# Kernel tuning notes

Hardware: AMD Instinct MI355X
Metric: run time of the kernel (lower is better)

## Reference

```python
import jax, jax.numpy as jnp
import numpy as np

HIDDEN = 2048
HEADS = 16
HEAD_DIM = HIDDEN // HEADS
NEG = -10000000000.0

def setup_inputs() -> dict:
    key = jax.random.key(0)
    k1, k2, k3 = jax.random.split(key, 3)
    x = jax.random.normal(k1, (2, 2048, HIDDEN), dtype=jnp.float32)
    # Dense kernels (flax convention: y = x @ W), lecun_normal-ish scaling
    w_qkv = jax.random.normal(k2, (HIDDEN, 3 * HIDDEN), dtype=jnp.float32) / np.sqrt(HIDDEN)
    w_out = jax.random.normal(k3, (HIDDEN, HIDDEN), dtype=jnp.float32) / np.sqrt(HIDDEN)
    return {"x": x, "w_qkv": w_qkv, "w_out": w_out}

def reference(x, w_qkv, w_out):
    b, s, _ = x.shape
    qkv = x @ w_qkv  # [b, s, 3*hidden]
    qkv = qkv.reshape(b, s, 3, HEADS, HEAD_DIM)
    q, k, v = qkv[:, :, 0], qkv[:, :, 1], qkv[:, :, 2]
    scale = jnp.sqrt(jnp.float32(HEAD_DIM)).astype(x.dtype)
    q = q / scale
    scores = jnp.einsum('bqhd,bkhd->bhqk', q, k)  # [b, h, s, s]
    causal_mask = jnp.arange(s)[:, None] >= jnp.arange(s)[None, :]
    scores = jnp.where(causal_mask[None, None], scores, NEG)
    attn = jax.nn.softmax(scores, axis=-1)
    out = jnp.einsum('bhqk,bkhd->bqhd', attn, v).reshape(b, s, HIDDEN)
    return out @ w_out
```

## Files before the change

### kernel.cpp

```cpp
#include <hip/hip_runtime.h>
#include <hip/hip_bf16.h>

typedef __attribute__((ext_vector_type(8))) short bf16x8;
typedef __attribute__((ext_vector_type(4))) float f32x4;
typedef unsigned short ushort_t;

#define HID 2048
#define QKVN 6144
#define SEQ 2048
#define NH 16
#define HD 128
#define QB 128
#define KVB 64

#define GLOBAL_AS __attribute__((address_space(1)))
#define LDS_AS __attribute__((address_space(3)))
typedef LDS_AS const char lds_char;

__device__ __forceinline__ void gload_lds16(const ushort_t* g, ushort_t* l) {
    __builtin_amdgcn_global_load_lds((const GLOBAL_AS unsigned int*)g,
                                     (LDS_AS unsigned int*)l, 16, 0, 0);
}

__device__ __forceinline__ bf16x8 dsr128(lds_char* p) {
    bf16x8 r;
    asm volatile("ds_read_b128 %0, %1" : "=v"(r) : "v"(p));
    return r;
}

__device__ __forceinline__ ushort_t f2b(float f) {
    union { float f; unsigned int u; } x; x.f = f;
    unsigned int r = x.u + 0x7fffu + ((x.u >> 16) & 1u);
    return (ushort_t)(r >> 16);
}

#define BARX() asm volatile("s_barrier" ::: "memory")
#define LGKM0() asm volatile("s_waitcnt lgkmcnt(0)" ::: "memory")
#define VMC6() asm volatile("s_waitcnt vmcnt(6)" ::: "memory")
#define VMC0() asm volatile("s_waitcnt vmcnt(0)" ::: "memory")

__global__ __launch_bounds__(256) void castbf(const float* __restrict__ in,
                                              ushort_t* __restrict__ out, int n) {
    int i = (blockIdx.x * 256 + threadIdx.x) * 8;
    if (i >= n) return;
    float4 a = *(const float4*)(in + i);
    float4 b = *(const float4*)(in + i + 4);
    union { ushort_t u[8]; uint4 v; } r;
    r.u[0] = f2b(a.x); r.u[1] = f2b(a.y); r.u[2] = f2b(a.z); r.u[3] = f2b(a.w);
    r.u[4] = f2b(b.x); r.u[5] = f2b(b.y); r.u[6] = f2b(b.z); r.u[7] = f2b(b.w);
    *(uint4*)(out + i) = r.v;
}

__global__ __launch_bounds__(256) void transcast(const float* __restrict__ in,
                                                 ushort_t* __restrict__ out,
                                                 int Kd, int Nd) {
    __shared__ float tile[32][33];
    int tx = threadIdx.x & 31, ty = threadIdx.x >> 5;
    int n0 = blockIdx.x * 32, k0 = blockIdx.y * 32;
    for (int j = 0; j < 4; j++)
        tile[ty + 8 * j][tx] = in[(size_t)(k0 + ty + 8 * j) * Nd + n0 + tx];
    __syncthreads();
    for (int j = 0; j < 4; j++)
        out[(size_t)(n0 + ty + 8 * j) * Kd + k0 + tx] = f2b(tile[tx][ty + 8 * j]);
}

__global__ __launch_bounds__(256) void transV(const ushort_t* __restrict__ qkvb,
                                              ushort_t* __restrict__ vT) {
    __shared__ ushort_t tile[32][33];
    int tx = threadIdx.x & 31, ty = threadIdx.x >> 5;
    int s0 = blockIdx.x * 32, d0 = blockIdx.y * 32;
    int bh = blockIdx.z; int b = bh >> 4, h = bh & 15;
    for (int j = 0; j < 4; j++)
        tile[ty + 8 * j][tx] =
            qkvb[(size_t)(b * SEQ + s0 + ty + 8 * j) * QKVN + 2 * HID + h * HD + d0 + tx];
    __syncthreads();
    for (int j = 0; j < 4; j++)
        vT[((size_t)bh * HD + d0 + ty + 8 * j) * SEQ + s0 + tx] = tile[tx][ty + 8 * j];
}

template <bool OUT_BF16>
__global__ __launch_bounds__(512, 1) void gemm4p(const ushort_t* __restrict__ A,
                                                 const ushort_t* __restrict__ BT,
                                                 void* __restrict__ C,
                                                 int M, int N, int K,
                                                 int scale_cols, float scale) {
    __shared__ __align__(16) ushort_t As[2][2][128 * 32];
    __shared__ __align__(16) ushort_t Bs[2][2][256 * 32];

    const int t = threadIdx.x;
    const int l = t & 63, w = t >> 6;
    const int wm = w >> 2, wn = w & 3;
    const int lr = l & 15, lg = l >> 4;

    const int nwg = gridDim.x;
    const int cpx = nwg >> 3;
    const int swb = (blockIdx.x & 7) * cpx + (blockIdx.x >> 3);
    const int NTN = N >> 8;
    const int m0 = (swb / NTN) << 7, n0 = (swb % NTN) << 8;

    const int NKT = K >> 6;
    const int NIT = NKT >> 1;

    f32x4 acc[4][4] = {};

#define STAGE_A(BUF, KK, KT)                                                    \
    do {                                                                        \
        const int r_ = t >> 2, g_ = t & 3;                                      \
        const int gc_ = ((KT) << 6) + ((KK) << 5) + ((g_ ^ (r_ & 3)) << 3);     \
        gload_lds16(A + (size_t)(m0 + r_) * K + gc_, &As[BUF][KK][t * 8]);      \
    } while (0)
#define STAGE_B(BUF, KK, KT)                                                        \
    do {                                                                            \
        _Pragma("unroll") for (int sx = 0; sx < 2; sx++) {                          \
            const int i_ = sx * 512 + t;                                            \
            const int r_ = i_ >> 2, g_ = i_ & 3;                                    \
            const int gc_ = ((KT) << 6) + ((KK) << 5) + ((g_ ^ (r_ & 3)) << 3);     \
            gload_lds16(BT + (size_t)(n0 + r_) * K + gc_, &Bs[BUF][KK][i_ * 8]);    \
        }                                                                           \
    } while (0)

#define PHASE(BUF, KK, STAGES)                                                  \
    {                                                                           \
        bf16x8 af[4], bfr[4];                                                   \
        lds_char* aB_ = (lds_char*)&As[BUF][KK][0];                             \
        lds_char* bB_ = (lds_char*)&Bs[BUF][KK][0];                             \
        const int co_ = (lg ^ (lr & 3)) << 4;                                   \
        _Pragma("unroll") for (int mi = 0; mi < 4; mi++)                        \
            af[mi] = dsr128(aB_ + (wm * 64 + mi * 16 + lr) * 64 + co_);         \
        _Pragma("unroll") for (int nn = 0; nn < 4; nn++)                        \
            bfr[nn] = dsr128(bB_ + (wn * 64 + nn * 16 + lr) * 64 + co_);        \
        STAGES;                                                                 \
        VMC6();                                                                 \
        BARX();                                                                 \
        LGKM0();                                                                \
        __builtin_amdgcn_sched_barrier(0);                                      \
        __builtin_amdgcn_s_setprio(1);                                          \
        _Pragma("unroll") for (int mi = 0; mi < 4; mi++)                        \
            _Pragma("unroll") for (int nn = 0; nn < 4; nn++)                    \
                acc[mi][nn] = __builtin_amdgcn_mfma_f32_16x16x32_bf16(          \
                    af[mi], bfr[nn], acc[mi][nn], 0, 0, 0);                     \
        __builtin_amdgcn_s_setprio(0);                                          \
        BARX();                                                                 \
    }

    STAGE_A(0, 0, 0); STAGE_B(0, 0, 0);
    STAGE_A(0, 1, 0); STAGE_B(0, 1, 0);
    STAGE_A(1, 0, 1); STAGE_B(1, 0, 1);
    VMC6();
    BARX();

    for (int it = 0; it < NIT; it++) {
        const int kt1 = 2 * it + 1;
        const int kt2 = min(2 * it + 2, NKT - 1);
        const int kt3 = min(2 * it + 3, NKT - 1);
        PHASE(0, 0, { STAGE_A(1, 1, kt1); STAGE_B(1, 1, kt1); });
        PHASE(0, 1, { STAGE_A(0, 0, kt2); STAGE_B(0, 0, kt2); });
        PHASE(1, 0, { STAGE_A(0, 1, kt2); STAGE_B(0, 1, kt2); });
        PHASE(1, 1, { STAGE_A(1, 0, kt3); STAGE_B(1, 0, kt3); });
    }
    VMC0();

#undef PHASE
#undef STAGE_A
#undef STAGE_B

#pragma unroll
    for (int mi = 0; mi < 4; mi++)
#pragma unroll
        for (int nn = 0; nn < 4; nn++) {
            const int row = m0 + wm * 64 + mi * 16 + lg * 4;
            const int col = n0 + wn * 64 + nn * 16 + lr;
            const float sc = (col < scale_cols) ? scale : 1.0f;
            const f32x4 v = acc[mi][nn];
#pragma unroll
            for (int j = 0; j < 4; j++) {
                if (OUT_BF16)
                    ((ushort_t*)C)[(size_t)(row + j) * N + col] = f2b(v[j] * sc);
                else
                    ((float*)C)[(size_t)(row + j) * N + col] = v[j] * sc;
            }
        }
}

__global__ __launch_bounds__(512, 1) void attn_fwd3(const ushort_t* __restrict__ qkvb,
                                                    const ushort_t* __restrict__ vT,
                                                    ushort_t* __restrict__ attnb) {
    __shared__ __align__(16) ushort_t Ks[2][64 * 128];
    __shared__ __align__(16) ushort_t Vs[2][128 * 64];
    __shared__ __align__(16) ushort_t Ps[8][16 * 64];

    const int t = threadIdx.x;
    const int l = t & 63, w = t >> 6;
    const int lr = l & 15, lg = l >> 4;
    const int pr = blockIdx.x, h = blockIdx.y, b = blockIdx.z;

    const ushort_t* kg = qkvb + (size_t)(b * SEQ) * QKVN + HID + h * HD;
    const ushort_t* vg = vT + (size_t)(b * NH + h) * HD * SEQ;

    char* PsB = (char*)Ps[w];
    const int pssz = ((lr & 7) ^ ((lr >> 3) << 1)) << 4;

    const int kcA = 2 * w, kcB = 2 * w + 1;
    const int krA = 8 * w + (l >> 4), krB = krA + 4;
    const int kcolA = ((l & 15) ^ (l >> 4)) << 3;
    const int kcolB = ((l & 15) ^ (4 + (l >> 4))) << 3;
    const int vrA = 16 * w + (l >> 3), vrB = vrA + 8;
    const int vcol = ((l & 7) ^ (l >> 3)) << 3;

    for (int seg = 0; seg < 2; seg++) {
        const int qt = (seg == 0) ? pr : 15 - pr;
        const int q0 = qt * QB;
        const int q0w = q0 + w * 16;
        const int NT = (q0 + QB) / KVB;

        bf16x8 qf[4];
        {
            const ushort_t* qb = qkvb + (size_t)(b * SEQ + q0w + lr) * QKVN + h * HD + lg * 8;
#pragma unroll
            for (int kc = 0; kc < 4; kc++) qf[kc] = *(const bf16x8*)(qb + kc * 32);
        }
        f32x4 o[8] = {};
        float m[4] = {-3e38f, -3e38f, -3e38f, -3e38f};
        float ls[4] = {0.f, 0.f, 0.f, 0.f};

        __syncthreads();
        gload_lds16(kg + (size_t)krA * QKVN + kcolA, &Ks[0][kcA * 512 + l * 8]);
        gload_lds16(kg + (size_t)krB * QKVN + kcolB, &Ks[0][kcB * 512 + l * 8]);
        gload_lds16(vg + (size_t)vrA * SEQ + vcol,   &Vs[0][kcA * 512 + l * 8]);
        gload_lds16(vg + (size_t)vrB * SEQ + vcol,   &Vs[0][kcB * 512 + l * 8]);

        for (int kt = 0; kt < NT; kt++) {
            const int kv0 = kt * KVB;
            __syncthreads();
            if (kt + 1 < NT) {
                const int nb = (kt + 1) & 1;
                const int nkv = kv0 + KVB;
                gload_lds16(kg + (size_t)(nkv + krA) * QKVN + kcolA, &Ks[nb][kcA * 512 + l * 8]);
                gload_lds16(kg + (size_t)(nkv + krB) * QKVN + kcolB, &Ks[nb][kcB * 512 + l * 8]);
                gload_lds16(vg + (size_t)vrA * SEQ + nkv + vcol,     &Vs[nb][kcA * 512 + l * 8]);
                gload_lds16(vg + (size_t)vrB * SEQ + nkv + vcol,     &Vs[nb][kcB * 512 + l * 8]);
            }
            if (kv0 > q0w + 15) continue;
            const char* KsB = (const char*)Ks[kt & 1];
            const char* VsB = (const char*)Vs[kt & 1];

            f32x4 s[4];
            const int rs = (lr & 7) << 4;
#pragma unroll
            for (int nf = 0; nf < 4; nf++) {
                const int r = nf * 16 + lr;
                s[nf] = (f32x4){0.f, 0.f, 0.f, 0.f};
#pragma unroll
                for (int kc = 0; kc < 4; kc++) {
                    bf16x8 kf = *(const bf16x8*)(KsB + r * 256 + ((kc * 64 + lg * 16) ^ rs));
                    s[nf] = __builtin_amdgcn_mfma_f32_16x16x32_bf16(qf[kc], kf, s[nf], 0, 0, 0);
                }
            }

            const bool diag = (kv0 + 63 > q0w);
            float tm[4];
#pragma unroll
            for (int j = 0; j < 4; j++) {
                if (diag) {
                    const int qpos = q0w + lg * 4 + j;
#pragma unroll
                    for (int nf = 0; nf < 4; nf++)
                        if (kv0 + nf * 16 + lr > qpos) s[nf][j] = -3e38f;
                }
                tm[j] = fmaxf(fmaxf(s[0][j], s[1][j]), fmaxf(s[2][j], s[3][j]));
#pragma unroll
                for (int mk = 1; mk < 16; mk <<= 1)
                    tm[j] = fmaxf(tm[j], __shfl_xor(tm[j], mk, 64));
            }

            float grow = fmaxf(fmaxf(tm[0] - m[0], tm[1] - m[1]),
                               fmaxf(tm[2] - m[2], tm[3] - m[3]));
            if (!__all(grow <= 8.0f)) {
#pragma unroll
                for (int j = 0; j < 4; j++) {
                    const float mn = fmaxf(m[j], tm[j]);
                    const float fac = exp2f((m[j] - mn) * 1.44269504f);
                    m[j] = mn; ls[j] *= fac;
#pragma unroll
                    for (int nf2 = 0; nf2 < 8; nf2++) o[nf2][j] *= fac;
                }
            }

#pragma unroll
            for (int j = 0; j < 4; j++) {
                const int row = lg * 4 + j;
                const int rsz = ((row & 7) ^ ((row >> 3) << 1)) << 4;
                float psum = 0.f;
#pragma unroll
                for (int nf = 0; nf < 4; nf++) {
                    float p = exp2f((s[nf][j] - m[j]) * 1.44269504f);
                    psum += p;
                    union { float f; unsigned u; } cv; cv.f = p;
                    *(ushort_t*)(PsB + row * 128 + ((nf * 32 + lr * 2) ^ rsz)) = (ushort_t)(cv.u >> 16);
                }
                ls[j] += psum;
            }

            bf16x8 pa0 = *(const bf16x8*)(PsB + lr * 128 + ((lg * 16) ^ pssz));
            bf16x8 pa1 = *(const bf16x8*)(PsB + lr * 128 + ((64 + lg * 16) ^ pssz));
#pragma unroll
            for (int nf2 = 0; nf2 < 8; nf2++) {
                const int vr2 = nf2 * 16 + lr;
                bf16x8 vb0 = *(const bf16x8*)(VsB + vr2 * 128 + ((lg * 16) ^ rs));
                bf16x8 vb1 = *(const bf16x8*)(VsB + vr2 * 128 + ((64 + lg * 16) ^ rs));
                o[nf2] = __builtin_amdgcn_mfma_f32_16x16x32_bf16(pa0, vb0, o[nf2], 0, 0, 0);
                o[nf2] = __builtin_amdgcn_mfma_f32_16x16x32_bf16(pa1, vb1, o[nf2], 0, 0, 0);
            }
        }

        float inv[4];
#pragma unroll
        for (int j = 0; j < 4; j++) {
            float sum = ls[j];
#pragma unroll
            for (int mk = 1; mk < 16; mk <<= 1) sum += __shfl_xor(sum, mk, 64);
            inv[j] = 1.0f / sum;
        }
        ushort_t* ob = attnb + (size_t)(b * SEQ + q0w) * HID + h * HD;
#pragma unroll
        for (int nf2 = 0; nf2 < 8; nf2++)
#pragma unroll
            for (int j = 0; j < 4; j++)
                ob[(size_t)(lg * 4 + j) * HID + nf2 * 16 + lr] = f2b(o[nf2][j] * inv[j]);
    }
}

extern "C" void kernel_launch(void* const* d_in, const int* in_sizes, int n_in,
                              void* d_out, int out_size, void* d_ws, size_t ws_size,
                              hipStream_t stream) {
    const float* x     = (const float*)d_in[0];
    const float* w_qkv = (const float*)d_in[1];
    const float* w_out = (const float*)d_in[2];
    float* out = (float*)d_out;

    char* ws = (char*)d_ws;
    ushort_t* xb    = (ushort_t*)(ws);
    ushort_t* wqkvT = (ushort_t*)(ws + 16777216);
    ushort_t* woutT = (ushort_t*)(ws + 41943040);
    ushort_t* qkvb  = (ushort_t*)(ws + 50331648);
    ushort_t* vT    = (ushort_t*)(ws + 100663296);
    ushort_t* attnb = (ushort_t*)(ws + 117440512);

    const int M = 2 * SEQ;

    castbf<<<(M * HID) / (256 * 8), 256, 0, stream>>>(x, xb, M * HID);
    transcast<<<dim3(QKVN / 32, HID / 32), 256, 0, stream>>>(w_qkv, wqkvT, HID, QKVN);
    transcast<<<dim3(HID / 32, HID / 32), 256, 0, stream>>>(w_out, woutT, HID, HID);

    gemm4p<true><<<(M / 128) * (QKVN / 256), 512, 0, stream>>>(
        xb, wqkvT, qkvb, M, QKVN, HID, HID, 0.08838834764831845f);

    transV<<<dim3(SEQ / 32, HD / 32, 2 * NH), 256, 0, stream>>>(qkvb, vT);

    attn_fwd3<<<dim3(8, NH, 2), 512, 0, stream>>>(qkvb, vT, attnb);

    gemm4p<false><<<(M / 128) * (HID / 256), 512, 0, stream>>>(
        attnb, woutT, out, M, HID, HID, 0, 1.0f);
}
```

Baseline: 282.9 us.

## Rewrite GEMM as triple-buffered register-prefetch pipeline with wider QKV tile

Replaces the two-stage, double-k-half GEMM with a three-slot LDS ring over 32-wide K steps. LDS fragment reads for the next step go into alternate register sets while the current step's MFMAs run, and each step issues only one barrier. The swizzle pattern is changed, and the QKV projection uses 384-wide N tiles (6 fragments per wave) to cut the tile count and raise reuse of A. This adds register pressure and LDS use, and the grid count for QKV (32*16=512 tiles) changes how evenly work spreads across CUs.

Measured after the change: 269.1 us. 1.05x faster.

```diff
diff --git a/kernel.cpp b/kernel.cpp
--- a/kernel.cpp
+++ b/kernel.cpp
@@ -36,7 +36,6 @@
 
 #define BARX() asm volatile("s_barrier" ::: "memory")
 #define LGKM0() asm volatile("s_waitcnt lgkmcnt(0)" ::: "memory")
-#define VMC6() asm volatile("s_waitcnt vmcnt(6)" ::: "memory")
 #define VMC0() asm volatile("s_waitcnt vmcnt(0)" ::: "memory")
 
 __global__ __launch_bounds__(256) void castbf(const float* __restrict__ in,
@@ -78,14 +77,14 @@
         vT[((size_t)bh * HD + d0 + ty + 8 * j) * SEQ + s0 + tx] = tile[tx][ty + 8 * j];
 }
 
-template <bool OUT_BF16>
-__global__ __launch_bounds__(512, 1) void gemm4p(const ushort_t* __restrict__ A,
+template <int NFRAG, bool OUT_BF16>
+__global__ __launch_bounds__(512, 1) void gemmpl(const ushort_t* __restrict__ A,
                                                  const ushort_t* __restrict__ BT,
                                                  void* __restrict__ C,
                                                  int M, int N, int K,
                                                  int scale_cols, float scale) {
-    __shared__ __align__(16) ushort_t As[2][2][128 * 32];
-    __shared__ __align__(16) ushort_t Bs[2][2][256 * 32];
+    __shared__ __align__(16) ushort_t As[3][128 * 32];
+    __shared__ __align__(16) ushort_t Bs[3][NFRAG * 64 * 32];
 
     const int t = threadIdx.x;
     const int l = t & 63, w = t >> 6;
@@ -95,83 +94,107 @@
     const int nwg = gridDim.x;
     const int cpx = nwg >> 3;
     const int swb = (blockIdx.x & 7) * cpx + (blockIdx.x >> 3);
-    const int NTN = N >> 8;
-    const int m0 = (swb / NTN) << 7, n0 = (swb % NTN) << 8;
-
-    const int NKT = K >> 6;
-    const int NIT = NKT >> 1;
-
-    f32x4 acc[4][4] = {};
-
-#define STAGE_A(BUF, KK, KT)                                                    \
+    const int BN = NFRAG * 64;
+    const int NTN = N / BN;
+    const int m0 = (swb / NTN) << 7, n0 = (swb % NTN) * BN;
+
+    const int NKT = K >> 5;
+
+    f32x4 acc[4][NFRAG] = {};
+    bf16x8 afA[4], bfA[NFRAG], afB[4], bfB[NFRAG];
+
+#define VMCL()                                                                      \
+    do { if constexpr (NFRAG == 6) asm volatile("s_waitcnt vmcnt(4)" ::: "memory"); \
+         else                      asm volatile("s_waitcnt vmcnt(3)" ::: "memory"); } while (0)
+#define VMC2L()                                                                     \
+    do { if constexpr (NFRAG == 6) asm volatile("s_waitcnt vmcnt(8)" ::: "memory"); \
+         else                      asm volatile("s_waitcnt vmcnt(6)" ::: "memory"); } while (0)
+
+#define STAGE_A(BUF, KT)                                                        \
     do {                                                                        \
         const int r_ = t >> 2, g_ = t & 3;                                      \
-        const int gc_ = ((KT) << 6) + ((KK) << 5) + ((g_ ^ (r_ & 3)) << 3);     \
-        gload_lds16(A + (size_t)(m0 + r_) * K + gc_, &As[BUF][KK][t * 8]);      \
+        const int gc_ = ((KT) << 5) + ((g_ ^ ((r_ >> 1) & 3)) << 3);            \
+        gload_lds16(A + (size_t)(m0 + r_) * K + gc_, &As[BUF][t * 8]);          \
     } while (0)
-#define STAGE_B(BUF, KK, KT)                                                        \
+#define STAGE_B(BUF, KT)                                                        \
+    do {                                                                        \
+        _Pragma("unroll") for (int sx = 0; sx < NFRAG / 2; sx++) {              \
+            const int i_ = sx * 512 + t;                                        \
+            const int r_ = i_ >> 2, g_ = i_ & 3;                                \
+            const int gc_ = ((KT) << 5) + ((g_ ^ ((r_ >> 1) & 3)) << 3);        \
+            gload_lds16(BT + (size_t)(n0 + r_) * K + gc_, &Bs[BUF][i_ * 8]);    \
+        }                                                                       \
+    } while (0)
+
+#define READS(AF, BF, BI)                                                           \
     do {                                                                            \
-        _Pragma("unroll") for (int sx = 0; sx < 2; sx++) {                          \
-            const int i_ = sx * 512 + t;                                            \
-            const int r_ = i_ >> 2, g_ = i_ & 3;                                    \
-            const int gc_ = ((KT) << 6) + ((KK) << 5) + ((g_ ^ (r_ & 3)) << 3);     \
-            gload_lds16(BT + (size_t)(n0 + r_) * K + gc_, &Bs[BUF][KK][i_ * 8]);    \
-        }                                                                           \
+        lds_char* aB_ = (lds_char*)&As[BI][0];                                      \
+        lds_char* bB_ = (lds_char*)&Bs[BI][0];                                      \
+        const int co_ = (lg ^ ((lr >> 1) & 3)) << 4;                                \
+        _Pragma("unroll") for (int mi = 0; mi < 4; mi++)                            \
+            AF[mi] = dsr128(aB_ + (wm * 64 + mi * 16 + lr) * 64 + co_);             \
+        _Pragma("unroll") for (int nj = 0; nj < NFRAG; nj++)                        \
+            BF[nj] = dsr128(bB_ + (wn * (NFRAG * 16) + nj * 16 + lr) * 64 + co_);   \
     } while (0)
 
-#define PHASE(BUF, KK, STAGES)                                                  \
+#define MFMAS(AF, BF)                                                           \
+    do {                                                                        \
+        __builtin_amdgcn_s_setprio(1);                                          \
+        _Pragma("unroll") for (int mi = 0; mi < 4; mi++)                        \
+            _Pragma("unroll") for (int nj = 0; nj < NFRAG; nj++)                \
+                acc[mi][nj] = __builtin_amdgcn_mfma_f32_16x16x32_bf16(          \
+                    AF[mi], BF[nj], acc[mi][nj], 0, 0, 0);                      \
+        __builtin_amdgcn_s_setprio(0);                                          \
+    } while (0)
+
+#define STEPX(AFU, BFU, AFV, BFV, BI, KT)                                       \
     {                                                                           \
-        bf16x8 af[4], bfr[4];                                                   \
-        lds_char* aB_ = (lds_char*)&As[BUF][KK][0];                             \
-        lds_char* bB_ = (lds_char*)&Bs[BUF][KK][0];                             \
-        const int co_ = (lg ^ (lr & 3)) << 4;                                   \
-        _Pragma("unroll") for (int mi = 0; mi < 4; mi++)                        \
-            af[mi] = dsr128(aB_ + (wm * 64 + mi * 16 + lr) * 64 + co_);         \
-        _Pragma("unroll") for (int nn = 0; nn < 4; nn++)                        \
-            bfr[nn] = dsr128(bB_ + (wn * 64 + nn * 16 + lr) * 64 + co_);        \
-        STAGES;                                                                 \
-        VMC6();                                                                 \
-        BARX();                                                                 \
         LGKM0();                                                                \
         __builtin_amdgcn_sched_barrier(0);                                      \
-        __builtin_amdgcn_s_setprio(1);                                          \
-        _Pragma("unroll") for (int mi = 0; mi < 4; mi++)                        \
-            _Pragma("unroll") for (int nn = 0; nn < 4; nn++)                    \
-                acc[mi][nn] = __builtin_amdgcn_mfma_f32_16x16x32_bf16(          \
-                    af[mi], bfr[nn], acc[mi][nn], 0, 0, 0);                     \
-        __builtin_amdgcn_s_setprio(0);                                          \
         BARX();                                                                 \
+        int nb_ = (BI) + 1; if (nb_ == 3) nb_ = 0;                              \
+        READS(AFV, BFV, nb_);                                                   \
+        const int st_ = min((KT) + 3, NKT - 1);                                 \
+        STAGE_A(BI, st_);                                                       \
+        STAGE_B(BI, st_);                                                       \
+        VMCL();                                                                 \
+        __builtin_amdgcn_sched_barrier(0);                                      \
+        MFMAS(AFU, BFU);                                                        \
     }
 
-    STAGE_A(0, 0, 0); STAGE_B(0, 0, 0);
-    STAGE_A(0, 1, 0); STAGE_B(0, 1, 0);
-    STAGE_A(1, 0, 1); STAGE_B(1, 0, 1);
-    VMC6();
+    STAGE_A(0, 0); STAGE_B(0, 0);
+    STAGE_A(1, 1); STAGE_B(1, 1);
+    STAGE_A(2, 2); STAGE_B(2, 2);
+    VMC2L();
     BARX();
-
-    for (int it = 0; it < NIT; it++) {
-        const int kt1 = 2 * it + 1;
-        const int kt2 = min(2 * it + 2, NKT - 1);
-        const int kt3 = min(2 * it + 3, NKT - 1);
-        PHASE(0, 0, { STAGE_A(1, 1, kt1); STAGE_B(1, 1, kt1); });
-        PHASE(0, 1, { STAGE_A(0, 0, kt2); STAGE_B(0, 0, kt2); });
-        PHASE(1, 0, { STAGE_A(0, 1, kt2); STAGE_B(0, 1, kt2); });
-        PHASE(1, 1, { STAGE_A(1, 0, kt3); STAGE_B(1, 0, kt3); });
+    READS(afA, bfA, 0);
+    VMCL();
+
+    int bi = 0;
+    for (int kt = 0; kt < NKT; kt += 2) {
+        STEPX(afA, bfA, afB, bfB, bi, kt);
+        int bi1 = bi + 1; if (bi1 == 3) bi1 = 0;
+        STEPX(afB, bfB, afA, bfA, bi1, kt + 1);
+        bi += 2; if (bi >= 3) bi -= 3;
     }
     VMC0();
 
-#undef PHASE
+#undef STEPX
+#undef MFMAS
+#undef READS
 #undef STAGE_A
 #undef STAGE_B
+#undef VMCL
+#undef VMC2L
 
 #pragma unroll
     for (int mi = 0; mi < 4; mi++)
 #pragma unroll
-        for (int nn = 0; nn < 4; nn++) {
+        for (int nj = 0; nj < NFRAG; nj++) {
             const int row = m0 + wm * 64 + mi * 16 + lg * 4;
-            const int col = n0 + wn * 64 + nn * 16 + lr;
+            const int col = n0 + wn * (NFRAG * 16) + nj * 16 + lr;
             const float sc = (col < scale_cols) ? scale : 1.0f;
-            const f32x4 v = acc[mi][nn];
+            const f32x4 v = acc[mi][nj];
 #pragma unroll
             for (int j = 0; j < 4; j++) {
                 if (OUT_BF16)
@@ -352,13 +375,13 @@
     transcast<<<dim3(QKVN / 32, HID / 32), 256, 0, stream>>>(w_qkv, wqkvT, HID, QKVN);
     transcast<<<dim3(HID / 32, HID / 32), 256, 0, stream>>>(w_out, woutT, HID, HID);
 
-    gemm4p<true><<<(M / 128) * (QKVN / 256), 512, 0, stream>>>(
+    gemmpl<6, true><<<(M / 128) * (QKVN / 384), 512, 0, stream>>>(
         xb, wqkvT, qkvb, M, QKVN, HID, HID, 0.08838834764831845f);
 
     transV<<<dim3(SEQ / 32, HD / 32, 2 * NH), 256, 0, stream>>>(qkvb, vT);
 
     attn_fwd3<<<dim3(8, NH, 2), 512, 0, stream>>>(qkvb, vT, attnb);
 
-    gemm4p<false><<<(M / 128) * (HID / 256), 512, 0, stream>>>(
+    gemmpl<4, false><<<(M / 128) * (HID / 256), 512, 0, stream>>>(
         attnb, woutT, out, M, HID, HID, 0, 1.0f);
 }
```
